# Performance work log

Measured on AMD Instinct MI355X. Metric: run time of the kernel, lower is better.

## Reference

```python
import jax, jax.numpy as jnp
import numpy as np

N_NODES = 100000
N_EDGES = 1600000
IN_FEAT = 128
HIDDEN = 128
N_CLASSES = 40


def setup_inputs() -> dict:
    key = jax.random.key(0)
    k1, k2, k3, k4 = jax.random.split(key, 4)
    x = jax.random.normal(k1, (N_NODES, IN_FEAT), dtype=jnp.float32)
    edge_index = jax.random.randint(k2, (2, N_EDGES), 0, N_NODES, dtype=jnp.int64)
    W1 = jax.random.normal(k3, (IN_FEAT, HIDDEN), dtype=jnp.float32) * (1.0 / np.sqrt(IN_FEAT))
    b1 = jnp.zeros((HIDDEN,), dtype=jnp.float32)
    W2 = jax.random.normal(k4, (HIDDEN, N_CLASSES), dtype=jnp.float32) * (1.0 / np.sqrt(HIDDEN))
    b2 = jnp.zeros((N_CLASSES,), dtype=jnp.float32)
    return {"x": x, "edge_index": edge_index, "W1": W1, "b1": b1, "W2": W2, "b2": b2}


def _gcn_conv(x, row, col, W, b, n_nodes):
    # x: [N, F_in] -> [N, F_out]; GCNConv: lin -> gather -> deg-norm -> scatter-add -> +bias
    h = x @ W  # dense transform first (PyG GCNConv order)
    # add self-loops
    loops = jnp.arange(n_nodes, dtype=row.dtype)
    row = jnp.concatenate([row, loops])
    col = jnp.concatenate([col, loops])
    # symmetric degree normalization: deg computed on destination (col)
    deg = jax.ops.segment_sum(jnp.ones_like(col, dtype=h.dtype), col, num_segments=n_nodes)
    dis = jnp.where(deg > 0, jax.lax.rsqrt(deg), 0.0)
    norm = dis[row] * dis[col]  # [E+N]
    msg = h[row] * norm[:, None]  # [E+N, F_out] gather + scale
    out = jax.ops.segment_sum(msg, col, num_segments=n_nodes)  # scatter-add
    return out + b


def reference(x, edge_index, W1, b1, W2, b2):
    row, col = edge_index[0], edge_index[1]
    n = x.shape[0]
    h = _gcn_conv(x, row, col, W1, b1, n)
    h = jax.nn.relu(h)
    # dropout p=0 / eval mode -> identity
    h = _gcn_conv(h, row, col, W2, b2, n)
    return jax.nn.log_softmax(h, axis=1)
```

## Files before the change

### kernel.cpp

```cpp
#include <hip/hip_runtime.h>
#include <hip/hip_bf16.h>
#include <math.h>

typedef unsigned short u16x8 __attribute__((ext_vector_type(8)));
typedef short s16x8 __attribute__((ext_vector_type(8)));
typedef float f32x4 __attribute__((ext_vector_type(4)));

#define BIN_TILE 4096
#define BCAP 8192

__device__ __forceinline__ float bf2f(unsigned int u) {
    union { unsigned int i; float f; } x;
    x.i = u << 16;
    return x.f;
}
__device__ __forceinline__ unsigned short f2bf(float f) {
    __hip_bfloat16 h = __float2bfloat16(f);
    return *reinterpret_cast<unsigned short*>(&h);
}

__global__ void bin_kernel(const int* __restrict__ row, const int* __restrict__ col,
                           int* __restrict__ bcnt, unsigned* __restrict__ tmp, int E, int NB) {
    __shared__ unsigned hist[512];
    int tid = threadIdx.x;
    int base = blockIdx.x * BIN_TILE;
    for (int i = tid; i < NB; i += 256) hist[i] = 0;
    __syncthreads();
#pragma unroll
    for (int i = 0; i < BIN_TILE / 256; i++) {
        int e = base + tid + i * 256;
        if (e < E) atomicAdd(&hist[col[e] >> 8], 1u);
    }
    __syncthreads();
    for (int i = tid; i < NB; i += 256) {
        unsigned h = hist[i];
        hist[i] = h ? (unsigned)atomicAdd(&bcnt[i], (int)h) : 0u;
    }
    __syncthreads();
#pragma unroll
    for (int i = 0; i < BIN_TILE / 256; i++) {
        int e = base + tid + i * 256;
        if (e < E) {
            int c = col[e], r = row[e];
            unsigned p = atomicAdd(&hist[c >> 8], 1u);
            tmp[(size_t)(c >> 8) * BCAP + p] = (unsigned)r | ((unsigned)(c & 255) << 20);
        }
    }
}

__global__ void bscan_kernel(const int* __restrict__ bcnt, int* __restrict__ boffs, int NB) {
    __shared__ int s[512];
    int tid = threadIdx.x;
    int v = (tid < NB) ? bcnt[tid] : 0;
    s[tid] = v;
    __syncthreads();
    for (int off = 1; off < 512; off <<= 1) {
        int t = (tid >= off) ? s[tid - off] : 0;
        __syncthreads();
        s[tid] += t;
        __syncthreads();
    }
    if (tid < NB) boffs[tid] = s[tid] - v;
    if (tid == NB - 1) boffs[NB] = s[tid];
}

__global__ void bucket_kernel(const unsigned* __restrict__ tmp, const int* __restrict__ bcnt,
                              const int* __restrict__ boffs, int* __restrict__ cnt,
                              int* __restrict__ offs, float* __restrict__ dis,
                              int* __restrict__ csr, int N) {
    __shared__ int cntS[256], curS[256], sA[256], sB[256];
    int b = blockIdx.x;
    int tid = threadIdx.x;
    size_t tbase = (size_t)b * BCAP;
    int ecnt = bcnt[b];
    int start = boffs[b];
    cntS[tid] = 0;
    __syncthreads();
    for (int i = tid; i < ecnt; i += 256)
        atomicAdd(&cntS[(tmp[tbase + i] >> 20) & 255], 1);
    __syncthreads();
    int myCnt = cntS[tid];
    sA[tid] = myCnt;
    __syncthreads();
    int* src = sA;
    int* dst = sB;
    for (int off = 1; off < 256; off <<= 1) {
        dst[tid] = src[tid] + ((tid >= off) ? src[tid - off] : 0);
        __syncthreads();
        int* t = src; src = dst; dst = t;
    }
    int excl = src[tid] - myCnt;
    int node = (b << 8) + tid;
    if (node < N) {
        cnt[node] = myCnt;
        offs[node] = start + excl;
        dis[node] = rsqrtf((float)myCnt + 1.0f);
    }
    curS[tid] = excl;
    __syncthreads();
    for (int i = tid; i < ecnt; i += 256) {
        unsigned u = tmp[tbase + i];
        int cl = (u >> 20) & 255;
        int p = atomicAdd(&curS[cl], 1);
        csr[start + p] = (int)(u & 0xFFFFFu);
    }
}

__global__ void scale_cvt_kernel(const float* __restrict__ x, const float* __restrict__ dis,
                                 unsigned short* __restrict__ xbs, int N) {
    long idx = (long)blockIdx.x * blockDim.x + threadIdx.x;
    long total8 = (long)(N + 1) * 16;
    if (idx >= total8) return;
    int i = (int)(idx >> 4);
    u16x8 o;
    if (i >= N) {
#pragma unroll
        for (int k = 0; k < 8; k++) o[k] = 0;
    } else {
        float d = dis[i];
        float4 a = ((const float4*)x)[2 * idx];
        float4 b = ((const float4*)x)[2 * idx + 1];
        o[0] = f2bf(d * a.x); o[1] = f2bf(d * a.y); o[2] = f2bf(d * a.z); o[3] = f2bf(d * a.w);
        o[4] = f2bf(d * b.x); o[5] = f2bf(d * b.y); o[6] = f2bf(d * b.z); o[7] = f2bf(d * b.w);
    }
    ((u16x8*)xbs)[idx] = o;
}

__global__ void zrow_kernel(unsigned* __restrict__ p32) {
    if (threadIdx.x < 32) p32[threadIdx.x] = 0;
}

__global__ void w1pack_kernel(const float* __restrict__ W, unsigned short* __restrict__ wp) {
    int t = blockIdx.x * blockDim.x + threadIdx.x;
    if (t >= 2048) return;
    int lane = t & 63, fc = t >> 6;
    int ct = fc >> 2, kc = fc & 3;
    int n = ct * 16 + (lane & 15);
    int k0 = kc * 32 + (lane >> 4) * 8;
    u16x8 o;
#pragma unroll
    for (int j = 0; j < 8; j++) o[j] = f2bf(W[(size_t)(k0 + j) * 128 + n]);
    ((u16x8*)wp)[t] = o;
}

__global__ void w2pack_kernel(const float* __restrict__ W, unsigned short* __restrict__ wp) {
    int t = blockIdx.x * blockDim.x + threadIdx.x;
    if (t >= 768) return;
    int lane = t & 63, fc = t >> 6;
    int ct = fc >> 2, kc = fc & 3;
    int n = ct * 16 + (lane & 15);
    int k0 = kc * 32 + (lane >> 4) * 8;
    u16x8 o;
#pragma unroll
    for (int j = 0; j < 8; j++) o[j] = (n < 40) ? f2bf(W[(size_t)(k0 + j) * 40 + n]) : (unsigned short)0;
    ((u16x8*)wp)[t] = o;
}

__global__ void gather1_kernel(const unsigned short* __restrict__ xbs, const int* __restrict__ offs,
                               const int* __restrict__ cnt, const int* __restrict__ csr,
                               const float* __restrict__ dis, unsigned short* __restrict__ xa, int N) {
    int node = blockIdx.x * 4 + (threadIdx.x >> 6);
    int lane = threadIdx.x & 63;
    if (node >= N) return;
    int off = offs[node], dg = cnt[node];
    int g = lane >> 4, c = lane & 15;
    const u16x8* XB = (const u16x8*)xbs;
    float acc[8] = {};
    int s0 = (g      < dg) ? csr[off + g]      : N;
    int s1 = (g + 4  < dg) ? csr[off + g + 4]  : N;
    int s2 = (g + 8  < dg) ? csr[off + g + 8]  : N;
    int s3 = (g + 12 < dg) ? csr[off + g + 12] : N;
    for (int j = 0; j < dg; j += 16) {
        int jb = j + 16;
        int t0 = (jb + g      < dg) ? csr[off + jb + g]      : N;
        int t1 = (jb + g + 4  < dg) ? csr[off + jb + g + 4]  : N;
        int t2 = (jb + g + 8  < dg) ? csr[off + jb + g + 8]  : N;
        int t3 = (jb + g + 12 < dg) ? csr[off + jb + g + 12] : N;
        u16x8 v0 = XB[(size_t)s0 * 16 + c];
        u16x8 v1 = XB[(size_t)s1 * 16 + c];
        u16x8 v2 = XB[(size_t)s2 * 16 + c];
        u16x8 v3 = XB[(size_t)s3 * 16 + c];
#pragma unroll
        for (int k = 0; k < 8; k++)
            acc[k] += (bf2f(v0[k]) + bf2f(v1[k])) + (bf2f(v2[k]) + bf2f(v3[k]));
        s0 = t0; s1 = t1; s2 = t2; s3 = t3;
    }
#pragma unroll
    for (int k = 0; k < 8; k++) {
        acc[k] += __shfl_xor(acc[k], 16);
        acc[k] += __shfl_xor(acc[k], 32);
    }
    float dc = dis[node];
    u16x8 xv = XB[(size_t)node * 16 + c];
    if (lane < 16) {
        u16x8 o;
#pragma unroll
        for (int k = 0; k < 8; k++) o[k] = f2bf(dc * (acc[k] + bf2f(xv[k])));
        ((u16x8*)xa)[(size_t)node * 16 + c] = o;
    }
}

__global__ __launch_bounds__(256) void mlp_kernel(const unsigned short* __restrict__ xa,
                                                  const unsigned short* __restrict__ w1p,
                                                  const unsigned short* __restrict__ w2p,
                                                  const float* __restrict__ b1,
                                                  const float* __restrict__ dis,
                                                  unsigned short* __restrict__ h2s, int N) {
    __shared__ unsigned short a1s[64][136];
    int wv = threadIdx.x >> 6;
    int l = threadIdx.x & 63;
    int row16 = l & 15, kg = l >> 4;
    int n0 = blockIdx.x * 64;
    int rbase = n0 + wv * 16;

    f32x4 acc[8];
#pragma unroll
    for (int ct = 0; ct < 8; ct++) acc[ct] = (f32x4)0.f;
    int r = rbase + row16;
    int rc = (r < N) ? r : (N - 1);
#pragma unroll
    for (int kc = 0; kc < 4; kc++) {
        s16x8 af = *(const s16x8*)(xa + (size_t)rc * 128 + kc * 32 + kg * 8);
#pragma unroll
        for (int ct = 0; ct < 8; ct++) {
            s16x8 bf = *(const s16x8*)(w1p + (size_t)((ct * 4 + kc) * 64 + l) * 8);
            acc[ct] = __builtin_amdgcn_mfma_f32_16x16x32_bf16(af, bf, acc[ct], 0, 0, 0);
        }
    }
#pragma unroll
    for (int ct = 0; ct < 8; ct++) {
        float bb = b1[ct * 16 + row16];
#pragma unroll
        for (int v = 0; v < 4; v++)
            a1s[wv * 16 + kg * 4 + v][ct * 16 + row16] = f2bf(fmaxf(acc[ct][v] + bb, 0.f));
    }
    __syncthreads();

    f32x4 acc2[3];
#pragma unroll
    for (int ct = 0; ct < 3; ct++) acc2[ct] = (f32x4)0.f;
#pragma unroll
    for (int kc = 0; kc < 4; kc++) {
        s16x8 af = *(const s16x8*)&a1s[wv * 16 + row16][kc * 32 + kg * 8];
#pragma unroll
        for (int ct = 0; ct < 3; ct++) {
            s16x8 bf = *(const s16x8*)(w2p + (size_t)((ct * 4 + kc) * 64 + l) * 8);
            acc2[ct] = __builtin_amdgcn_mfma_f32_16x16x32_bf16(af, bf, acc2[ct], 0, 0, 0);
        }
    }
#pragma unroll
    for (int v = 0; v < 4; v++) {
        int rr = rbase + kg * 4 + v;
        if (rr < N) {
            float d = dis[rr];
#pragma unroll
            for (int ct = 0; ct < 3; ct++)
                h2s[(size_t)rr * 64 + ct * 16 + row16] = f2bf(d * acc2[ct][v]);
        }
    }
}

__global__ void gather2_kernel(const unsigned short* __restrict__ h2s, const int* __restrict__ offs,
                               const int* __restrict__ cnt, const int* __restrict__ csr,
                               const float* __restrict__ dis, const float* __restrict__ b2,
                               float* __restrict__ out, int N) {
    int node = blockIdx.x * 4 + (threadIdx.x >> 6);
    int lane = threadIdx.x & 63;
    if (node >= N) return;
    int off = offs[node], dg = cnt[node];
    int c = lane % 20;
    int g = lane / 20;
    if (g == 3) g = 2;
    const unsigned* H32 = (const unsigned*)h2s;
    float a0 = 0.f, a1 = 0.f;
    int s0 = (g     < dg) ? csr[off + g]     : N;
    int s1 = (g + 3 < dg) ? csr[off + g + 3] : N;
    int s2 = (g + 6 < dg) ? csr[off + g + 6] : N;
    int s3 = (g + 9 < dg) ? csr[off + g + 9] : N;
    for (int j = 0; j < dg; j += 12) {
        int jb = j + 12;
        int t0 = (jb + g     < dg) ? csr[off + jb + g]     : N;
        int t1 = (jb + g + 3 < dg) ? csr[off + jb + g + 3] : N;
        int t2 = (jb + g + 6 < dg) ? csr[off + jb + g + 6] : N;
        int t3 = (jb + g + 9 < dg) ? csr[off + jb + g + 9] : N;
        unsigned u0 = H32[(size_t)s0 * 32 + c];
        unsigned u1 = H32[(size_t)s1 * 32 + c];
        unsigned u2 = H32[(size_t)s2 * 32 + c];
        unsigned u3 = H32[(size_t)s3 * 32 + c];
        a0 += (bf2f(u0 & 0xffffu) + bf2f(u1 & 0xffffu)) + (bf2f(u2 & 0xffffu) + bf2f(u3 & 0xffffu));
        a1 += (bf2f(u0 >> 16) + bf2f(u1 >> 16)) + (bf2f(u2 >> 16) + bf2f(u3 >> 16));
        s0 = t0; s1 = t1; s2 = t2; s3 = t3;
    }
    float b0 = __shfl(a0, lane + 20);
    float b1_ = __shfl(a0, lane + 40);
    a0 = a0 + b0 + b1_;
    b0 = __shfl(a1, lane + 20);
    b1_ = __shfl(a1, lane + 40);
    a1 = a1 + b0 + b1_;

    float dc = dis[node];
    bool act = lane < 20;
    unsigned u = H32[(size_t)node * 32 + c];
    float v0 = act ? (dc * (a0 + bf2f(u & 0xffffu)) + b2[2 * c]) : -INFINITY;
    float v1 = act ? (dc * (a1 + bf2f(u >> 16)) + b2[2 * c + 1]) : -INFINITY;
    float m = fmaxf(v0, v1);
#pragma unroll
    for (int o = 32; o > 0; o >>= 1) m = fmaxf(m, __shfl_xor(m, o));
    float ex = act ? (__expf(v0 - m) + __expf(v1 - m)) : 0.f;
#pragma unroll
    for (int o = 32; o > 0; o >>= 1) ex += __shfl_xor(ex, o);
    float ls = __logf(ex);
    if (act) {
        float2 o2 = make_float2(v0 - m - ls, v1 - m - ls);
        ((float2*)(out + (size_t)node * 40))[c] = o2;
    }
}

extern "C" void kernel_launch(void* const* d_in, const int* in_sizes, int n_in,
                              void* d_out, int out_size, void* d_ws, size_t ws_size,
                              hipStream_t stream) {
    const float* x  = (const float*)d_in[0];
    const int*   ei = (const int*)d_in[1];
    const float* W1 = (const float*)d_in[2];
    const float* b1 = (const float*)d_in[3];
    const float* W2 = (const float*)d_in[4];
    const float* b2 = (const float*)d_in[5];
    float* out = (float*)d_out;

    const int N = in_sizes[0] / 128;
    const int E = in_sizes[1] / 2;
    const int* row = ei;
    const int* col = ei + E;

    const int Npad = (N + 511) & ~511;
    const int Epad = (E + 511) & ~511;
    const int NB = (N + 255) >> 8;

    int* cnt      = (int*)d_ws;
    int* offs     = cnt + Npad;
    int* bcnt     = offs + Npad;
    int* boffs    = bcnt + 512;
    int* csr      = boffs + 1024;
    unsigned* tmp = (unsigned*)(csr + Epad);
    float* dis    = (float*)(tmp + (size_t)NB * BCAP);
    unsigned short* w1p = (unsigned short*)(dis + Npad);
    unsigned short* w2p = w1p + 16384;
    unsigned short* xbs = w2p + 8192;
    unsigned short* xa  = xbs + (size_t)(N + 1) * 128;
    unsigned short* h2s = xa + (size_t)N * 128;

    hipMemsetAsync(bcnt, 0, 512 * sizeof(int), stream);
    bin_kernel<<<(E + BIN_TILE - 1) / BIN_TILE, 256, 0, stream>>>(row, col, bcnt, tmp, E, NB);
    bscan_kernel<<<1, 512, 0, stream>>>(bcnt, boffs, NB);
    bucket_kernel<<<NB, 256, 0, stream>>>(tmp, bcnt, boffs, cnt, offs, dis, csr, N);

    w1pack_kernel<<<8, 256, 0, stream>>>(W1, w1p);
    w2pack_kernel<<<3, 256, 0, stream>>>(W2, w2p);
    zrow_kernel<<<1, 64, 0, stream>>>((unsigned*)(h2s + (size_t)N * 64));
    {
        long total8 = (long)(N + 1) * 16;
        scale_cvt_kernel<<<(int)((total8 + 255) / 256), 256, 0, stream>>>(x, dis, xbs, N);
    }

    gather1_kernel<<<(N + 3) / 4, 256, 0, stream>>>(xbs, offs, cnt, csr, dis, xa, N);

    mlp_kernel<<<(N + 63) / 64, 256, 0, stream>>>(xa, w1p, w2p, b1, dis, h2s, N);

    gather2_kernel<<<(N + 3) / 4, 256, 0, stream>>>(h2s, offs, cnt, csr, dis, b2, out, N);
}
```

Baseline: 192.1 us.

## Fold bucket scan into bucket kernel, merge prep kernels, widen gather2 loads

Removes the single-block bscan kernel: each bucket block now sums the preceding bucket counts itself with a shared-memory reduction. The two weight-pack kernels and the zero-row kernel become one prep kernel, cutting launch count from three to one. gather2 now has each lane load four bf16 values (ushort4) instead of two, so 10 lanes cover a row and 6 edge groups run in parallel, giving more edges per wave iteration. The trade-off is redundant prefix work in every bucket block and an extra shuffle-reduction stage in gather2.

```diff
diff --git a/kernel.cpp b/kernel.cpp
--- a/kernel.cpp
+++ b/kernel.cpp
@@ -48,34 +48,27 @@
     }
 }
 
-__global__ void bscan_kernel(const int* __restrict__ bcnt, int* __restrict__ boffs, int NB) {
-    __shared__ int s[512];
-    int tid = threadIdx.x;
-    int v = (tid < NB) ? bcnt[tid] : 0;
-    s[tid] = v;
-    __syncthreads();
-    for (int off = 1; off < 512; off <<= 1) {
-        int t = (tid >= off) ? s[tid - off] : 0;
-        __syncthreads();
-        s[tid] += t;
-        __syncthreads();
-    }
-    if (tid < NB) boffs[tid] = s[tid] - v;
-    if (tid == NB - 1) boffs[NB] = s[tid];
-}
-
 __global__ void bucket_kernel(const unsigned* __restrict__ tmp, const int* __restrict__ bcnt,
-                              const int* __restrict__ boffs, int* __restrict__ cnt,
-                              int* __restrict__ offs, float* __restrict__ dis,
-                              int* __restrict__ csr, int N) {
+                              int* __restrict__ cnt, int* __restrict__ offs,
+                              float* __restrict__ dis, int* __restrict__ csr, int N, int NB) {
     __shared__ int cntS[256], curS[256], sA[256], sB[256];
     int b = blockIdx.x;
     int tid = threadIdx.x;
     size_t tbase = (size_t)b * BCAP;
+
+    cntS[tid] = 0;
+    int partial = 0;
+    if (tid < b) partial += bcnt[tid];
+    if (tid + 256 < b) partial += bcnt[tid + 256];
+    sA[tid] = partial;
+    __syncthreads();
+    for (int s = 128; s > 0; s >>= 1) {
+        if (tid < s) sA[tid] += sA[tid + s];
+        __syncthreads();
+    }
+    int start = sA[0];
     int ecnt = bcnt[b];
-    int start = boffs[b];
-    cntS[tid] = 0;
-    __syncthreads();
+
     for (int i = tid; i < ecnt; i += 256)
         atomicAdd(&cntS[(tmp[tbase + i] >> 20) & 255], 1);
     __syncthreads();
@@ -126,34 +119,33 @@
     ((u16x8*)xbs)[idx] = o;
 }
 
-__global__ void zrow_kernel(unsigned* __restrict__ p32) {
-    if (threadIdx.x < 32) p32[threadIdx.x] = 0;
-}
-
-__global__ void w1pack_kernel(const float* __restrict__ W, unsigned short* __restrict__ wp) {
-    int t = blockIdx.x * blockDim.x + threadIdx.x;
-    if (t >= 2048) return;
-    int lane = t & 63, fc = t >> 6;
-    int ct = fc >> 2, kc = fc & 3;
-    int n = ct * 16 + (lane & 15);
-    int k0 = kc * 32 + (lane >> 4) * 8;
-    u16x8 o;
-#pragma unroll
-    for (int j = 0; j < 8; j++) o[j] = f2bf(W[(size_t)(k0 + j) * 128 + n]);
-    ((u16x8*)wp)[t] = o;
-}
-
-__global__ void w2pack_kernel(const float* __restrict__ W, unsigned short* __restrict__ wp) {
-    int t = blockIdx.x * blockDim.x + threadIdx.x;
-    if (t >= 768) return;
-    int lane = t & 63, fc = t >> 6;
-    int ct = fc >> 2, kc = fc & 3;
-    int n = ct * 16 + (lane & 15);
-    int k0 = kc * 32 + (lane >> 4) * 8;
-    u16x8 o;
-#pragma unroll
-    for (int j = 0; j < 8; j++) o[j] = (n < 40) ? f2bf(W[(size_t)(k0 + j) * 40 + n]) : (unsigned short)0;
-    ((u16x8*)wp)[t] = o;
+__global__ void prep_kernel(const float* __restrict__ W1, const float* __restrict__ W2,
+                            unsigned short* __restrict__ w1p, unsigned short* __restrict__ w2p,
+                            unsigned* __restrict__ h2z) {
+    int bid = blockIdx.x, tid = threadIdx.x;
+    if (bid < 8) {
+        int t = bid * 256 + tid;
+        int lane = t & 63, fc = t >> 6;
+        int ct = fc >> 2, kc = fc & 3;
+        int n = ct * 16 + (lane & 15);
+        int k0 = kc * 32 + (lane >> 4) * 8;
+        u16x8 o;
+#pragma unroll
+        for (int j = 0; j < 8; j++) o[j] = f2bf(W1[(size_t)(k0 + j) * 128 + n]);
+        ((u16x8*)w1p)[t] = o;
+    } else if (bid < 11) {
+        int t = (bid - 8) * 256 + tid;
+        int lane = t & 63, fc = t >> 6;
+        int ct = fc >> 2, kc = fc & 3;
+        int n = ct * 16 + (lane & 15);
+        int k0 = kc * 32 + (lane >> 4) * 8;
+        u16x8 o;
+#pragma unroll
+        for (int j = 0; j < 8; j++) o[j] = (n < 40) ? f2bf(W2[(size_t)(k0 + j) * 40 + n]) : (unsigned short)0;
+        ((u16x8*)w2p)[t] = o;
+    } else {
+        if (tid < 32) h2z[tid] = 0;
+    }
 }
 
 __global__ void gather1_kernel(const unsigned short* __restrict__ xbs, const int* __restrict__ offs,
@@ -268,51 +260,63 @@
     int lane = threadIdx.x & 63;
     if (node >= N) return;
     int off = offs[node], dg = cnt[node];
-    int c = lane % 20;
-    int g = lane / 20;
-    if (g == 3) g = 2;
-    const unsigned* H32 = (const unsigned*)h2s;
-    float a0 = 0.f, a1 = 0.f;
-    int s0 = (g     < dg) ? csr[off + g]     : N;
-    int s1 = (g + 3 < dg) ? csr[off + g + 3] : N;
-    int s2 = (g + 6 < dg) ? csr[off + g + 6] : N;
-    int s3 = (g + 9 < dg) ? csr[off + g + 9] : N;
-    for (int j = 0; j < dg; j += 12) {
-        int jb = j + 12;
-        int t0 = (jb + g     < dg) ? csr[off + jb + g]     : N;
-        int t1 = (jb + g + 3 < dg) ? csr[off + jb + g + 3] : N;
-        int t2 = (jb + g + 6 < dg) ? csr[off + jb + g + 6] : N;
-        int t3 = (jb + g + 9 < dg) ? csr[off + jb + g + 9] : N;
-        unsigned u0 = H32[(size_t)s0 * 32 + c];
-        unsigned u1 = H32[(size_t)s1 * 32 + c];
-        unsigned u2 = H32[(size_t)s2 * 32 + c];
-        unsigned u3 = H32[(size_t)s3 * 32 + c];
-        a0 += (bf2f(u0 & 0xffffu) + bf2f(u1 & 0xffffu)) + (bf2f(u2 & 0xffffu) + bf2f(u3 & 0xffffu));
-        a1 += (bf2f(u0 >> 16) + bf2f(u1 >> 16)) + (bf2f(u2 >> 16) + bf2f(u3 >> 16));
+    int c = lane % 10;
+    int g = lane / 10;
+    if (g > 5) g = 5;
+    const ushort4* H4 = (const ushort4*)h2s;
+    float a0 = 0.f, a1 = 0.f, a2 = 0.f, a3 = 0.f;
+    int s0 = (g      < dg) ? csr[off + g]      : N;
+    int s1 = (g + 6  < dg) ? csr[off + g + 6]  : N;
+    int s2 = (g + 12 < dg) ? csr[off + g + 12] : N;
+    int s3 = (g + 18 < dg) ? csr[off + g + 18] : N;
+    for (int j = 0; j < dg; j += 24) {
+        int jb = j + 24;
+        int t0 = (jb + g      < dg) ? csr[off + jb + g]      : N;
+        int t1 = (jb + g + 6  < dg) ? csr[off + jb + g + 6]  : N;
+        int t2 = (jb + g + 12 < dg) ? csr[off + jb + g + 12] : N;
+        int t3 = (jb + g + 18 < dg) ? csr[off + jb + g + 18] : N;
+        ushort4 u0 = H4[(size_t)s0 * 16 + c];
+        ushort4 u1 = H4[(size_t)s1 * 16 + c];
+        ushort4 u2 = H4[(size_t)s2 * 16 + c];
+        ushort4 u3 = H4[(size_t)s3 * 16 + c];
+        a0 += (bf2f(u0.x) + bf2f(u1.x)) + (bf2f(u2.x) + bf2f(u3.x));
+        a1 += (bf2f(u0.y) + bf2f(u1.y)) + (bf2f(u2.y) + bf2f(u3.y));
+        a2 += (bf2f(u0.z) + bf2f(u1.z)) + (bf2f(u2.z) + bf2f(u3.z));
+        a3 += (bf2f(u0.w) + bf2f(u1.w)) + (bf2f(u2.w) + bf2f(u3.w));
         s0 = t0; s1 = t1; s2 = t2; s3 = t3;
     }
-    float b0 = __shfl(a0, lane + 20);
-    float b1_ = __shfl(a0, lane + 40);
-    a0 = a0 + b0 + b1_;
-    b0 = __shfl(a1, lane + 20);
-    b1_ = __shfl(a1, lane + 40);
-    a1 = a1 + b0 + b1_;
-
+    float t;
+    t = __shfl(a0, lane + 30); a0 += t;
+    t = __shfl(a1, lane + 30); a1 += t;
+    t = __shfl(a2, lane + 30); a2 += t;
+    t = __shfl(a3, lane + 30); a3 += t;
+    float p, q;
+    p = __shfl(a0, lane + 10); q = __shfl(a0, lane + 20); a0 += p + q;
+    p = __shfl(a1, lane + 10); q = __shfl(a1, lane + 20); a1 += p + q;
+    p = __shfl(a2, lane + 10); q = __shfl(a2, lane + 20); a2 += p + q;
+    p = __shfl(a3, lane + 10); q = __shfl(a3, lane + 20); a3 += p + q;
+
+    bool act = lane < 10;
     float dc = dis[node];
-    bool act = lane < 20;
-    unsigned u = H32[(size_t)node * 32 + c];
-    float v0 = act ? (dc * (a0 + bf2f(u & 0xffffu)) + b2[2 * c]) : -INFINITY;
-    float v1 = act ? (dc * (a1 + bf2f(u >> 16)) + b2[2 * c + 1]) : -INFINITY;
-    float m = fmaxf(v0, v1);
+    ushort4 uv = H4[(size_t)node * 16 + c];
+    float4 bb = ((const float4*)b2)[c];
+    float v0 = -INFINITY, v1 = -INFINITY, v2 = -INFINITY, v3 = -INFINITY;
+    if (act) {
+        v0 = dc * (a0 + bf2f(uv.x)) + bb.x;
+        v1 = dc * (a1 + bf2f(uv.y)) + bb.y;
+        v2 = dc * (a2 + bf2f(uv.z)) + bb.z;
+        v3 = dc * (a3 + bf2f(uv.w)) + bb.w;
+    }
+    float m = fmaxf(fmaxf(v0, v1), fmaxf(v2, v3));
 #pragma unroll
     for (int o = 32; o > 0; o >>= 1) m = fmaxf(m, __shfl_xor(m, o));
-    float ex = act ? (__expf(v0 - m) + __expf(v1 - m)) : 0.f;
+    float ex = act ? (__expf(v0 - m) + __expf(v1 - m) + __expf(v2 - m) + __expf(v3 - m)) : 0.f;
 #pragma unroll
     for (int o = 32; o > 0; o >>= 1) ex += __shfl_xor(ex, o);
     float ls = __logf(ex);
     if (act) {
-        float2 o2 = make_float2(v0 - m - ls, v1 - m - ls);
-        ((float2*)(out + (size_t)node * 40))[c] = o2;
+        float4 o4 = make_float4(v0 - m - ls, v1 - m - ls, v2 - m - ls, v3 - m - ls);
+        ((float4*)(out + (size_t)node * 40))[c] = o4;
     }
 }
 
@@ -339,8 +343,7 @@
     int* cnt      = (int*)d_ws;
     int* offs     = cnt + Npad;
     int* bcnt     = offs + Npad;
-    int* boffs    = bcnt + 512;
-    int* csr      = boffs + 1024;
+    int* csr      = bcnt + 1024;
     unsigned* tmp = (unsigned*)(csr + Epad);
     float* dis    = (float*)(tmp + (size_t)NB * BCAP);
     unsigned short* w1p = (unsigned short*)(dis + Npad);
@@ -351,12 +354,9 @@
 
     hipMemsetAsync(bcnt, 0, 512 * sizeof(int), stream);
     bin_kernel<<<(E + BIN_TILE - 1) / BIN_TILE, 256, 0, stream>>>(row, col, bcnt, tmp, E, NB);
-    bscan_kernel<<<1, 512, 0, stream>>>(bcnt, boffs, NB);
-    bucket_kernel<<<NB, 256, 0, stream>>>(tmp, bcnt, boffs, cnt, offs, dis, csr, N);
-
-    w1pack_kernel<<<8, 256, 0, stream>>>(W1, w1p);
-    w2pack_kernel<<<3, 256, 0, stream>>>(W2, w2p);
-    zrow_kernel<<<1, 64, 0, stream>>>((unsigned*)(h2s + (size_t)N * 64));
+    bucket_kernel<<<NB, 256, 0, stream>>>(tmp, bcnt, cnt, offs, dis, csr, N, NB);
+
+    prep_kernel<<<12, 256, 0, stream>>>(W1, W2, w1p, w2p, (unsigned*)(h2s + (size_t)N * 64));
     {
         long total8 = (long)(N + 1) * 16;
         scale_cvt_kernel<<<(int)((total8 + 255) / 256), 256, 0, stream>>>(x, dis, xbs, N);
```

Result: faster. 180.8 us (-5.9%).
